# Kernel tuning notes

Measured on AMD Instinct MI355X. Metric: run time of the kernel, lower is better.

## Reference

```python
import jax, jax.numpy as jnp
import numpy as np

NEG_SLOPE = 0.01  # F.leaky_relu default in GATLayer.edge_attention
N_NODES = 50000
N_EDGES = 1600000
IN_DIM = 128
HEADS = 8
D_HEAD = 16  # out_dim / head_num = 128 / 8


def setup_inputs() -> dict:
    key = jax.random.key(0)
    ks = jax.random.split(key, 9)
    # glorot-ish scales for linear projections and attention vectors
    w_scale = (2.0 / (IN_DIM + D_HEAD)) ** 0.5
    a_scale = (2.0 / (2 * D_HEAD + 1)) ** 0.5
    return {
        "x": jax.random.normal(ks[0], (N_NODES, IN_DIM), dtype=jnp.float32),
        "src": jax.random.randint(ks[1], (N_EDGES,), 0, N_NODES, dtype=jnp.int32),
        "dst": jax.random.randint(ks[2], (N_EDGES,), 0, N_NODES, dtype=jnp.int32),
        "W1": jax.random.normal(ks[3], (HEADS, IN_DIM, D_HEAD), dtype=jnp.float32) * w_scale,
        "a1_src": jax.random.normal(ks[4], (HEADS, D_HEAD), dtype=jnp.float32) * a_scale,
        "a1_dst": jax.random.normal(ks[5], (HEADS, D_HEAD), dtype=jnp.float32) * a_scale,
        "W2": jax.random.normal(ks[6], (HEADS, IN_DIM, D_HEAD), dtype=jnp.float32) * w_scale,
        "a2_src": jax.random.normal(ks[7], (HEADS, D_HEAD), dtype=jnp.float32) * a_scale,
        "a2_dst": jax.random.normal(ks[8], (HEADS, D_HEAD), dtype=jnp.float32) * a_scale,
    }


def gat_multihead(h, src, dst, W, a_src, a_dst, num_nodes):
    """One MultiHeadLayer(GATLayer) with concat merge. h: [N, Din]."""
    z = jnp.einsum("nd,hdk->nhk", h, W)            # [N,H,Dh] per-head projection
    # attn_fc(cat(z_src, z_dst)) == a_src . z_src + a_dst . z_dst
    s_src = jnp.einsum("nhk,hk->nh", z, a_src)      # [N,H]
    s_dst = jnp.einsum("nhk,hk->nh", z, a_dst)      # [N,H]
    e = jax.nn.leaky_relu(s_src[src] + s_dst[dst], NEG_SLOPE)  # [E,H]
    # segment softmax over incoming edges of each dst node
    e_max = jax.ops.segment_max(e, dst, num_segments=num_nodes)          # [N,H]
    e_max = jnp.where(jnp.isfinite(e_max), e_max, 0.0)                   # empty segments
    w = jnp.exp(e - e_max[dst])                                          # [E,H]
    denom = jax.ops.segment_sum(w, dst, num_segments=num_nodes)          # [N,H]
    msg = w[:, :, None] * z[src]                                         # [E,H,Dh]
    num = jax.ops.segment_sum(msg, dst, num_segments=num_nodes)          # [N,H,Dh]
    out = num / jnp.where(denom == 0.0, 1.0, denom)[:, :, None]
    return out.reshape(num_nodes, -1)                                    # concat heads -> [N, H*Dh]


def reference(x, src, dst, W1, a1_src, a1_dst, W2, a2_src, a2_dst):
    n = x.shape[0]
    h = gat_multihead(x, src, dst, W1, a1_src, a1_dst, n)
    h = jax.nn.elu(h)
    h = gat_multihead(h, src, dst, W2, a2_src, a2_dst, n)
    return h
```

## Files before the change

kernel.cpp:

```cpp
#include <hip/hip_runtime.h>
#include <hip/hip_bf16.h>

#define N_NODES 50000
#define N_EDGES 1600000
#define NEG_SLOPE 0.01f
#define WPAD 136

#define NBKT 256
#define BKTW 196
#define NBLK1 200
#define CHUNK1 8000

typedef _Float16 v8h __attribute__((ext_vector_type(8)));
typedef _Float16 v2h __attribute__((ext_vector_type(2)));
typedef float v4f __attribute__((ext_vector_type(4)));

__global__ __launch_bounds__(256) void proj_mfma_kernel(
    const float* __restrict__ x,
    const float* __restrict__ W,
    _Float16* __restrict__ z)
{
    __shared__ _Float16 Wl[128 * WPAD];

    const int t = threadIdx.x;
    for (int i = t; i < 16384; i += 256) {
        const int h = i >> 11, k = (i >> 4) & 127, col = i & 15;
        Wl[(h * 16 + col) * WPAD + k] = (_Float16)W[i];
    }
    __syncthreads();

    const int wid = t >> 6;
    const int l   = t & 63;
    const int lc  = l & 15;
    const int kg  = l >> 4;

    const int nwaves = gridDim.x * 4;
    for (int tile = blockIdx.x * 4 + wid; tile < N_NODES / 16; tile += nwaves) {
        const int n0 = tile * 16;
        v4f acc[8];
#pragma unroll
        for (int ht = 0; ht < 8; ht++) acc[ht] = (v4f)0.f;

#pragma unroll
        for (int kb = 0; kb < 4; kb++) {
            const float4* xp = (const float4*)&x[(n0 + lc) * 128 + kb * 32 + kg * 8];
            const float4 xa = xp[0];
            const float4 xb = xp[1];
            v8h a;
            a[0] = (_Float16)xa.x; a[1] = (_Float16)xa.y;
            a[2] = (_Float16)xa.z; a[3] = (_Float16)xa.w;
            a[4] = (_Float16)xb.x; a[5] = (_Float16)xb.y;
            a[6] = (_Float16)xb.z; a[7] = (_Float16)xb.w;
#pragma unroll
            for (int ht = 0; ht < 8; ht++) {
                const v8h b = *(const v8h*)&Wl[(ht * 16 + lc) * WPAD + kb * 32 + kg * 8];
                acc[ht] = __builtin_amdgcn_mfma_f32_16x16x32_f16(a, b, acc[ht], 0, 0, 0);
            }
        }

        _Float16* zp = &z[(n0 + 4 * kg) * 128 + lc];
#pragma unroll
        for (int ht = 0; ht < 8; ht++)
#pragma unroll
            for (int i = 0; i < 4; i++)
                zp[i * 128 + ht * 16] = (_Float16)acc[ht][i];
    }
}

__global__ __launch_bounds__(256) void score_kernel(
    const _Float16* __restrict__ z,
    const float* __restrict__ a_src, const float* __restrict__ a_dst,
    float* __restrict__ s_src, float* __restrict__ s_dst)
{
    __shared__ float asl[128], adl[128];
    const int t = threadIdx.x;
    if (t < 128) { asl[t] = a_src[t]; adl[t] = a_dst[t]; }
    __syncthreads();

    const int idx = blockIdx.x * 256 + t;
    if (idx >= N_NODES * 8) return;
    const int n = idx >> 3, h = idx & 7;

    const v8h z0 = *(const v8h*)&z[n * 128 + h * 16];
    const v8h z1 = *(const v8h*)&z[n * 128 + h * 16 + 8];
    float ss = 0.f, sd = 0.f;
#pragma unroll
    for (int j = 0; j < 8; j++) {
        ss = fmaf((float)z0[j], asl[h * 16 + j], ss);
        sd = fmaf((float)z0[j], adl[h * 16 + j], sd);
    }
#pragma unroll
    for (int j = 0; j < 8; j++) {
        ss = fmaf((float)z1[j], asl[h * 16 + 8 + j], ss);
        sd = fmaf((float)z1[j], adl[h * 16 + 8 + j], sd);
    }
    s_src[idx] = ss;
    s_dst[idx] = sd;
}

__global__ __launch_bounds__(256) void hist_bucket_kernel(
    const int* __restrict__ dst, int* __restrict__ bh)
{
    __shared__ int lhist[NBKT];
    const int t = threadIdx.x, blk = blockIdx.x;
    lhist[t] = 0;
    __syncthreads();
    const int e0 = blk * CHUNK1, e1 = e0 + CHUNK1;
    for (int e = e0 + t; e < e1; e += 256)
        atomicAdd(&lhist[(unsigned)dst[e] / BKTW], 1);
    __syncthreads();
    bh[t * NBLK1 + blk] = lhist[t];
}

__global__ __launch_bounds__(256) void scan_buckets_kernel(
    int* __restrict__ bh, int* __restrict__ btotal)
{
    __shared__ int sb[256];
    const int t = threadIdx.x, b = blockIdx.x;
    const int v = (t < NBLK1) ? bh[b * NBLK1 + t] : 0;
    sb[t] = v;
    __syncthreads();
    int x = v;
    for (int off = 1; off < 256; off <<= 1) {
        const int add = (t >= off) ? sb[t - off] : 0;
        __syncthreads();
        x += add;
        sb[t] = x;
        __syncthreads();
    }
    if (t < NBLK1) bh[b * NBLK1 + t] = x - v;
    if (t == 255) btotal[b] = x;
}

__global__ __launch_bounds__(256) void scan_totals_kernel(
    const int* __restrict__ btotal, int* __restrict__ bstart)
{
    __shared__ int sb[256];
    const int t = threadIdx.x;
    const int v = btotal[t];
    sb[t] = v;
    __syncthreads();
    int x = v;
    for (int off = 1; off < 256; off <<= 1) {
        const int add = (t >= off) ? sb[t - off] : 0;
        __syncthreads();
        x += add;
        sb[t] = x;
        __syncthreads();
    }
    bstart[t] = x - v;
    if (t == 255) bstart[256] = x;
}

__global__ __launch_bounds__(256) void scatter_bucket_kernel(
    const int* __restrict__ src, const int* __restrict__ dst,
    const int* __restrict__ bh, const int* __restrict__ bstart,
    int* __restrict__ gbuf)
{
    __shared__ int lbase[NBKT];
    __shared__ int lcur[NBKT];
    const int t = threadIdx.x, blk = blockIdx.x;
    lbase[t] = bstart[t] + bh[t * NBLK1 + blk];
    lcur[t] = 0;
    __syncthreads();
    const int e0 = blk * CHUNK1, e1 = e0 + CHUNK1;
    for (int e = e0 + t; e < e1; e += 256) {
        const int d = dst[e];
        const unsigned b = (unsigned)d / BKTW;
        const int ld = d - (int)b * BKTW;
        const int r = atomicAdd(&lcur[b], 1);
        gbuf[lbase[b] + r] = (ld << 16) | src[e];
    }
}

__global__ __launch_bounds__(256) void sort_bucket_kernel(
    const int* __restrict__ gbuf, const int* __restrict__ bstart,
    int* __restrict__ perm, int* __restrict__ rowp)
{
    __shared__ int lhist[NBKT];
    __shared__ int lscan[NBKT];
    __shared__ int lcur[NBKT];
    const int t = threadIdx.x, b = blockIdx.x;
    const int base = bstart[b];
    const int cnt  = bstart[b + 1] - base;
    const int n0   = b * BKTW;

    lhist[t] = 0;
    lcur[t] = 0;
    __syncthreads();
    for (int i = t; i < cnt; i += 256)
        atomicAdd(&lhist[gbuf[base + i] >> 16], 1);
    __syncthreads();

    const int v = lhist[t];
    lscan[t] = v;
    __syncthreads();
    int x = v;
    for (int off = 1; off < 256; off <<= 1) {
        const int add = (t >= off) ? lscan[t - off] : 0;
        __syncthreads();
        x += add;
        lscan[t] = x;
        __syncthreads();
    }
    const int excl = x - v;
    __syncthreads();
    lscan[t] = excl;

    const int n = n0 + t;
    if (t < BKTW && n < N_NODES) rowp[n] = base + excl;
    if (b == NBKT - 1 && t == 0) rowp[N_NODES] = bstart[NBKT];
    __syncthreads();

    for (int i = t; i < cnt; i += 256) {
        const int e = gbuf[base + i];
        const int ld = e >> 16;
        const int r = atomicAdd(&lcur[ld], 1);
        perm[base + lscan[ld] + r] = e & 0xFFFF;
    }
}

__global__ __launch_bounds__(128) void gather_kernel(
    const int* __restrict__ row_ptr, const int* __restrict__ perm,
    const _Float16* __restrict__ z,
    const float* __restrict__ s_src, const float* __restrict__ s_dst,
    float* __restrict__ out, const int apply_elu)
{
    __shared__ int   se_l[2][8];
    __shared__ float w_l[2][8][8];

    const int t  = threadIdx.x;
    const int wv = t >> 6;
    const int l  = t & 63;
    const int n  = blockIdx.x * 2 + wv;

    const int h8 = l & 7;
    const int je = l >> 3;
    const int c0 = 2 * l;
    const int h  = l >> 3;

    const int start = row_ptr[n];
    const int end   = row_ptr[n + 1];
    const float sd  = s_dst[n * 8 + h8];

    float acc0 = 0.f, acc1 = 0.f, wsum = 0.f;

    int   se_r = 0;
    float w_r  = 0.f;
    {
        const int j = start + je;
        if (j < end) {
            se_r = perm[j];
            float s = s_src[se_r * 8 + h8] + sd;
            s = s > 0.f ? s : NEG_SLOPE * s;
            w_r = __expf(s);
        }
    }

    for (int j0 = start; j0 < end; j0 += 8) {
        if (h8 == 0) se_l[wv][je] = se_r;
        w_l[wv][je][h8] = w_r;

        int   se_n = 0;
        float w_n  = 0.f;
        {
            const int j = j0 + 8 + je;
            if (j < end) {
                se_n = perm[j];
                float s = s_src[se_n * 8 + h8] + sd;
                s = s > 0.f ? s : NEG_SLOPE * s;
                w_n = __expf(s);
            }
        }

#pragma unroll
        for (int j = 0; j < 8; j++) {
            const float w  = w_l[wv][j][h];
            const int   se = se_l[wv][j];
            const v2h   zv = *(const v2h*)&z[se * 128 + c0];
            wsum += w;
            acc0 = fmaf(w, (float)zv[0], acc0);
            acc1 = fmaf(w, (float)zv[1], acc1);
        }

        se_r = se_n;
        w_r  = w_n;
    }

    const float inv = (wsum > 0.f) ? 1.f / wsum : 0.f;
    float o0 = acc0 * inv;
    float o1 = acc1 * inv;
    if (apply_elu) {
        o0 = o0 > 0.f ? o0 : expm1f(o0);
        o1 = o1 > 0.f ? o1 : expm1f(o1);
    }
    *(float2*)&out[n * 128 + c0] = make_float2(o0, o1);
}

extern "C" void kernel_launch(void* const* d_in, const int* in_sizes, int n_in,
                              void* d_out, int out_size, void* d_ws, size_t ws_size,
                              hipStream_t stream) {
    const float* x    = (const float*)d_in[0];
    const int*   src  = (const int*)d_in[1];
    const int*   dst  = (const int*)d_in[2];
    const float* W1   = (const float*)d_in[3];
    const float* a1s  = (const float*)d_in[4];
    const float* a1d  = (const float*)d_in[5];
    const float* W2   = (const float*)d_in[6];
    const float* a2s  = (const float*)d_in[7];
    const float* a2d  = (const float*)d_in[8];
    float* out = (float*)d_out;

    char* p = (char*)d_ws;
    _Float16* z  = (_Float16*)p;  p += (size_t)N_NODES * 128 * 2;
    float* ssrc  = (float*)p;     p += (size_t)N_NODES * 8 * 4;
    float* sdst  = (float*)p;     p += (size_t)N_NODES * 8 * 4;
    int*   rowp  = (int*)p;       p += ((size_t)N_NODES + 4) * 4;
    int*   bh    = (int*)p;       p += (size_t)NBKT * NBLK1 * 4;
    int*   btot  = (int*)p;       p += (size_t)NBKT * 4;
    int*   bstart= (int*)p;       p += ((size_t)NBKT + 4) * 4;
    int*   gbuf  = (int*)p;       p += (size_t)N_EDGES * 4;
    int*   perm  = (int*)p;       p += (size_t)N_EDGES * 4;

    const int PROJ_GRID  = 391;
    const int SCORE_GRID = (N_NODES * 8 + 255) / 256;

    hist_bucket_kernel<<<NBLK1, 256, 0, stream>>>(dst, bh);
    scan_buckets_kernel<<<NBKT, 256, 0, stream>>>(bh, btot);
    scan_totals_kernel<<<1, 256, 0, stream>>>(btot, bstart);
    scatter_bucket_kernel<<<NBLK1, 256, 0, stream>>>(src, dst, bh, bstart, gbuf);
    sort_bucket_kernel<<<NBKT, 256, 0, stream>>>(gbuf, bstart, perm, rowp);

    proj_mfma_kernel<<<PROJ_GRID, 256, 0, stream>>>(x, W1, z);
    score_kernel<<<SCORE_GRID, 256, 0, stream>>>(z, a1s, a1d, ssrc, sdst);
    gather_kernel<<<N_NODES / 2, 128, 0, stream>>>(rowp, perm, z, ssrc, sdst, out, 1);

    proj_mfma_kernel<<<PROJ_GRID, 256, 0, stream>>>(out, W2, z);
    score_kernel<<<SCORE_GRID, 256, 0, stream>>>(z, a2s, a2d, ssrc, sdst);
    gather_kernel<<<N_NODES / 2, 128, 0, stream>>>(rowp, perm, z, ssrc, sdst, out, 0);
}
```

Measured before the change: 218.8 us.

## Split gather across column slices and edge groups with shuffle reduction

Restructures the aggregation kernel so each wave handles one node's 32-column slice, with lanes split into four edge groups that each process two edges per iteration. A final xor-shuffle reduction combines the partial sums. This removes the LDS broadcast of edge indices and weights and raises the number of waves in flight, increasing memory-level parallelism. In exchange, the edge indices, source scores and exponentials are recomputed once per slice, four times per node.

New measurement: 467.7 us. 2.14x slower.

```diff
diff --git a/kernel.cpp b/kernel.cpp
--- a/kernel.cpp
+++ b/kernel.cpp
@@ -220,81 +220,91 @@
     }
 }
 
-__global__ __launch_bounds__(128) void gather_kernel(
+__global__ __launch_bounds__(256) void gather_kernel(
     const int* __restrict__ row_ptr, const int* __restrict__ perm,
     const _Float16* __restrict__ z,
     const float* __restrict__ s_src, const float* __restrict__ s_dst,
     float* __restrict__ out, const int apply_elu)
 {
-    __shared__ int   se_l[2][8];
-    __shared__ float w_l[2][8][8];
-
-    const int t  = threadIdx.x;
-    const int wv = t >> 6;
-    const int l  = t & 63;
-    const int n  = blockIdx.x * 2 + wv;
-
-    const int h8 = l & 7;
-    const int je = l >> 3;
-    const int c0 = 2 * l;
-    const int h  = l >> 3;
+    const int g     = blockIdx.x;
+    const int slice = g & 3;
+    const int group = g >> 2;
+    const int wv    = threadIdx.x >> 6;
+    const int l     = threadIdx.x & 63;
+    const int n     = group * 4 + wv;
+
+    const int q  = l >> 4;
+    const int ci = l & 15;
+    const int c0 = slice * 32 + ci * 2;
+    const int h  = c0 >> 4;
 
     const int start = row_ptr[n];
     const int end   = row_ptr[n + 1];
-    const float sd  = s_dst[n * 8 + h8];
+    const float sd  = s_dst[n * 8 + h];
 
     float acc0 = 0.f, acc1 = 0.f, wsum = 0.f;
 
-    int   se_r = 0;
-    float w_r  = 0.f;
+    int se_a = 0, se_b = 0;
+    float w_a = 0.f, w_b = 0.f;
     {
-        const int j = start + je;
-        if (j < end) {
-            se_r = perm[j];
-            float s = s_src[se_r * 8 + h8] + sd;
+        const int ja = start + q, jb = start + q + 4;
+        if (ja < end) {
+            se_a = perm[ja];
+            float s = s_src[se_a * 8 + h] + sd;
             s = s > 0.f ? s : NEG_SLOPE * s;
-            w_r = __expf(s);
+            w_a = __expf(s);
+        }
+        if (jb < end) {
+            se_b = perm[jb];
+            float s = s_src[se_b * 8 + h] + sd;
+            s = s > 0.f ? s : NEG_SLOPE * s;
+            w_b = __expf(s);
         }
     }
 
     for (int j0 = start; j0 < end; j0 += 8) {
-        if (h8 == 0) se_l[wv][je] = se_r;
-        w_l[wv][je][h8] = w_r;
-
-        int   se_n = 0;
-        float w_n  = 0.f;
+        const v2h za = *(const v2h*)&z[se_a * 128 + c0];
+        const v2h zb = *(const v2h*)&z[se_b * 128 + c0];
+        const float wa = w_a, wb = w_b;
+
+        se_a = 0; se_b = 0; w_a = 0.f; w_b = 0.f;
         {
-            const int j = j0 + 8 + je;
-            if (j < end) {
-                se_n = perm[j];
-                float s = s_src[se_n * 8 + h8] + sd;
+            const int ja = j0 + 8 + q, jb = j0 + 12 + q;
+            if (ja < end) {
+                se_a = perm[ja];
+                float s = s_src[se_a * 8 + h] + sd;
                 s = s > 0.f ? s : NEG_SLOPE * s;
-                w_n = __expf(s);
+                w_a = __expf(s);
             }
-        }
-
-#pragma unroll
-        for (int j = 0; j < 8; j++) {
-            const float w  = w_l[wv][j][h];
-            const int   se = se_l[wv][j];
-            const v2h   zv = *(const v2h*)&z[se * 128 + c0];
-            wsum += w;
-            acc0 = fmaf(w, (float)zv[0], acc0);
-            acc1 = fmaf(w, (float)zv[1], acc1);
-        }
-
-        se_r = se_n;
-        w_r  = w_n;
-    }
-
-    const float inv = (wsum > 0.f) ? 1.f / wsum : 0.f;
-    float o0 = acc0 * inv;
-    float o1 = acc1 * inv;
-    if (apply_elu) {
-        o0 = o0 > 0.f ? o0 : expm1f(o0);
-        o1 = o1 > 0.f ? o1 : expm1f(o1);
-    }
-    *(float2*)&out[n * 128 + c0] = make_float2(o0, o1);
+            if (jb < end) {
+                se_b = perm[jb];
+                float s = s_src[se_b * 8 + h] + sd;
+                s = s > 0.f ? s : NEG_SLOPE * s;
+                w_b = __expf(s);
+            }
+        }
+
+        wsum += wa + wb;
+        acc0 = fmaf(wa, (float)za[0], acc0);
+        acc1 = fmaf(wa, (float)za[1], acc1);
+        acc0 = fmaf(wb, (float)zb[0], acc0);
+        acc1 = fmaf(wb, (float)zb[1], acc1);
+    }
+
+    acc0 += __shfl_xor(acc0, 16); acc0 += __shfl_xor(acc0, 32);
+    acc1 += __shfl_xor(acc1, 16); acc1 += __shfl_xor(acc1, 32);
+    wsum += __shfl_xor(wsum, 16); wsum += __shfl_xor(wsum, 32);
+
+    if (l < 16) {
+        const float inv = (wsum > 0.f) ? 1.f / wsum : 0.f;
+        float o0 = acc0 * inv;
+        float o1 = acc1 * inv;
+        if (apply_elu) {
+            o0 = o0 > 0.f ? o0 : expm1f(o0);
+            o1 = o1 > 0.f ? o1 : expm1f(o1);
+        }
+        *(float2*)&out[n * 128 + c0] = make_float2(o0, o1);
+    }
 }
 
 extern "C" void kernel_launch(void* const* d_in, const int* in_sizes, int n_in,
@@ -322,8 +332,9 @@
     int*   gbuf  = (int*)p;       p += (size_t)N_EDGES * 4;
     int*   perm  = (int*)p;       p += (size_t)N_EDGES * 4;
 
-    const int PROJ_GRID  = 391;
-    const int SCORE_GRID = (N_NODES * 8 + 255) / 256;
+    const int PROJ_GRID   = 391;
+    const int SCORE_GRID  = (N_NODES * 8 + 255) / 256;
+    const int GATHER_GRID = (N_NODES / 4) * 4;
 
     hist_bucket_kernel<<<NBLK1, 256, 0, stream>>>(dst, bh);
     scan_buckets_kernel<<<NBKT, 256, 0, stream>>>(bh, btot);
@@ -333,9 +344,9 @@
 
     proj_mfma_kernel<<<PROJ_GRID, 256, 0, stream>>>(x, W1, z);
     score_kernel<<<SCORE_GRID, 256, 0, stream>>>(z, a1s, a1d, ssrc, sdst);
-    gather_kernel<<<N_NODES / 2, 128, 0, stream>>>(rowp, perm, z, ssrc, sdst, out, 1);
+    gather_kernel<<<GATHER_GRID, 256, 0, stream>>>(rowp, perm, z, ssrc, sdst, out, 1);
 
     proj_mfma_kernel<<<PROJ_GRID, 256, 0, stream>>>(out, W2, z);
     score_kernel<<<SCORE_GRID, 256, 0, stream>>>(z, a2s, a2d, ssrc, sdst);
-    gather_kernel<<<N_NODES / 2, 128, 0, stream>>>(rowp, perm, z, ssrc, sdst, out, 0);
-}
+    gather_kernel<<<GATHER_GRID, 256, 0, stream>>>(rowp, perm, z, ssrc, sdst, out, 0);
+}
```

## Split edge softmax weights into a separate kernel stored as bf16 per edge

Applied to the files above, without the earlier changes.

Computes the per-edge exp attention weights in a new edge_weight_kernel and writes them to a bf16 buffer in CSR order. The gather kernel then reads the weights and perm directly instead of computing them and exchanging them through LDS with a software-prefetch pipeline. Block size goes from 2 to 4 nodes per block. This adds an extra launch per layer plus a 25.6MB write and read of weights, and bf16 rounding of the weights lowers precision. Each lane in gather now loads perm and the weight redundantly.

Result: slower. 256.6 us (+17.3%).

```diff
diff --git a/kernel.cpp b/kernel.cpp
--- a/kernel.cpp
+++ b/kernel.cpp
@@ -220,74 +220,67 @@
     }
 }
 
-__global__ __launch_bounds__(128) void gather_kernel(
+__global__ __launch_bounds__(256) void edge_weight_kernel(
+    const int* __restrict__ rowp, const int* __restrict__ perm,
+    const float* __restrict__ s_src, const float* __restrict__ s_dst,
+    __hip_bfloat16* __restrict__ wperm)
+{
+    const int wv = threadIdx.x >> 6;
+    const int l  = threadIdx.x & 63;
+    const int n  = blockIdx.x * 4 + wv;
+
+    const int e8 = l >> 3;
+    const int h8 = l & 7;
+
+    const int start = rowp[n];
+    const int end   = rowp[n + 1];
+    const float sd  = s_dst[n * 8 + h8];
+
+    for (int j0 = start; j0 < end; j0 += 8) {
+        const int jj = j0 + e8;
+        if (jj < end) {
+            const int se = perm[jj];
+            float s = s_src[se * 8 + h8] + sd;
+            s = s > 0.f ? s : NEG_SLOPE * s;
+            wperm[jj * 8 + h8] = __float2bfloat16(__expf(s));
+        }
+    }
+}
+
+__global__ __launch_bounds__(256) void gather_kernel(
     const int* __restrict__ row_ptr, const int* __restrict__ perm,
+    const __hip_bfloat16* __restrict__ wperm,
     const _Float16* __restrict__ z,
-    const float* __restrict__ s_src, const float* __restrict__ s_dst,
     float* __restrict__ out, const int apply_elu)
 {
-    __shared__ int   se_l[2][8];
-    __shared__ float w_l[2][8][8];
-
-    const int t  = threadIdx.x;
-    const int wv = t >> 6;
-    const int l  = t & 63;
-    const int n  = blockIdx.x * 2 + wv;
-
-    const int h8 = l & 7;
-    const int je = l >> 3;
+    const int wv = threadIdx.x >> 6;
+    const int l  = threadIdx.x & 63;
+    const int n  = blockIdx.x * 4 + wv;
+
     const int c0 = 2 * l;
     const int h  = l >> 3;
 
     const int start = row_ptr[n];
     const int end   = row_ptr[n + 1];
-    const float sd  = s_dst[n * 8 + h8];
 
     float acc0 = 0.f, acc1 = 0.f, wsum = 0.f;
 
-    int   se_r = 0;
-    float w_r  = 0.f;
-    {
-        const int j = start + je;
-        if (j < end) {
-            se_r = perm[j];
-            float s = s_src[se_r * 8 + h8] + sd;
-            s = s > 0.f ? s : NEG_SLOPE * s;
-            w_r = __expf(s);
-        }
-    }
-
     for (int j0 = start; j0 < end; j0 += 8) {
-        if (h8 == 0) se_l[wv][je] = se_r;
-        w_l[wv][je][h8] = w_r;
-
-        int   se_n = 0;
-        float w_n  = 0.f;
-        {
-            const int j = j0 + 8 + je;
-            if (j < end) {
-                se_n = perm[j];
-                float s = s_src[se_n * 8 + h8] + sd;
-                s = s > 0.f ? s : NEG_SLOPE * s;
-                w_n = __expf(s);
-            }
-        }
-
-#pragma unroll
-        for (int j = 0; j < 8; j++) {
-            const float w  = w_l[wv][j][h];
-            const int   se = se_l[wv][j];
-            const v2h   zv = *(const v2h*)&z[se * 128 + c0];
+#pragma unroll
+        for (int k = 0; k < 8; k++) {
+            const int jr = j0 + k;
+            const int jj = (jr < end) ? jr : end - 1;
+            const int se = perm[jj];
+            float w = __bfloat162float(wperm[jj * 8 + h]);
+            w = (jr < end) ? w : 0.f;
+            const v2h zv = *(const v2h*)&z[se * 128 + c0];
             wsum += w;
             acc0 = fmaf(w, (float)zv[0], acc0);
             acc1 = fmaf(w, (float)zv[1], acc1);
         }
-
-        se_r = se_n;
-        w_r  = w_n;
-    }
-
-    const float inv = (wsum > 0.f) ? 1.f / wsum : 0.f;
+    }
+
+    const float inv = (end > start) ? 1.f / wsum : 0.f;
     float o0 = acc0 * inv;
     float o1 = acc1 * inv;
     if (apply_elu) {
@@ -313,6 +306,7 @@
 
     char* p = (char*)d_ws;
     _Float16* z  = (_Float16*)p;  p += (size_t)N_NODES * 128 * 2;
+    __hip_bfloat16* wperm = (__hip_bfloat16*)p; p += (size_t)N_EDGES * 8 * 2;
     float* ssrc  = (float*)p;     p += (size_t)N_NODES * 8 * 4;
     float* sdst  = (float*)p;     p += (size_t)N_NODES * 8 * 4;
     int*   rowp  = (int*)p;       p += ((size_t)N_NODES + 4) * 4;
@@ -322,8 +316,9 @@
     int*   gbuf  = (int*)p;       p += (size_t)N_EDGES * 4;
     int*   perm  = (int*)p;       p += (size_t)N_EDGES * 4;
 
-    const int PROJ_GRID  = 391;
-    const int SCORE_GRID = (N_NODES * 8 + 255) / 256;
+    const int PROJ_GRID   = 391;
+    const int SCORE_GRID  = (N_NODES * 8 + 255) / 256;
+    const int NODE4_GRID  = N_NODES / 4;
 
     hist_bucket_kernel<<<NBLK1, 256, 0, stream>>>(dst, bh);
     scan_buckets_kernel<<<NBKT, 256, 0, stream>>>(bh, btot);
@@ -333,9 +328,11 @@
 
     proj_mfma_kernel<<<PROJ_GRID, 256, 0, stream>>>(x, W1, z);
     score_kernel<<<SCORE_GRID, 256, 0, stream>>>(z, a1s, a1d, ssrc, sdst);
-    gather_kernel<<<N_NODES / 2, 128, 0, stream>>>(rowp, perm, z, ssrc, sdst, out, 1);
+    edge_weight_kernel<<<NODE4_GRID, 256, 0, stream>>>(rowp, perm, ssrc, sdst, wperm);
+    gather_kernel<<<NODE4_GRID, 256, 0, stream>>>(rowp, perm, wperm, z, out, 1);
 
     proj_mfma_kernel<<<PROJ_GRID, 256, 0, stream>>>(out, W2, z);
     score_kernel<<<SCORE_GRID, 256, 0, stream>>>(z, a2s, a2d, ssrc, sdst);
-    gather_kernel<<<N_NODES / 2, 128, 0, stream>>>(rowp, perm, z, ssrc, sdst, out, 0);
-}
+    edge_weight_kernel<<<NODE4_GRID, 256, 0, stream>>>(rowp, perm, ssrc, sdst, wperm);
+    gather_kernel<<<NODE4_GRID, 256, 0, stream>>>(rowp, perm, wperm, z, out, 0);
+}
```
